# Performance work log

Hardware: AMD Instinct MI355X
Metric: run time of the kernel (lower is better)

## Reference

```python
import jax, jax.numpy as jnp
import numpy as np

N = 50000      # nodes
E = 1600000    # edges (avg degree 32)
D = 128        # node_feat_size
G = 128        # graph_feat_size (must equal D for BatchNorm1d to match MLP out)
EPS = 1e-5
NEG_SLOPE = 0.01  # LeakyReLU default


def setup_inputs() -> dict:
    key = jax.random.key(0)
    ks = jax.random.split(key, 10)
    p = lambda k, sh: jax.random.normal(k, sh, dtype=jnp.float32) * 0.05
    return {
        "node_feats": jax.random.normal(ks[0], (N, D), dtype=jnp.float32),
        "src": jax.random.randint(ks[1], (E,), 0, N, dtype=jnp.int32),
        "dst": jax.random.randint(ks[2], (E,), 0, N, dtype=jnp.int32),
        # project_edge: Linear(2D -> 1); split weight into dst/src halves
        "we_dst": p(ks[3], (D,)),
        "we_src": p(ks[4], (D,)),
        "be": jnp.zeros((), jnp.float32),
        # project_node: Linear(D -> G)
        "w_proj": p(ks[5], (D, G)),
        "b_proj": jnp.zeros((G,), jnp.float32),
        # MPL: Linear(G+D -> D), ReLU, Linear(D -> D)
        "w1": p(ks[6], (G + D, D)),
        "b1": jnp.zeros((D,), jnp.float32),
        "w2": p(ks[7], (D, D)),
        "b2": jnp.zeros((D,), jnp.float32),
        # BatchNorm1d(G) affine params (training-mode batch stats)
        "gamma": jnp.ones((G,), jnp.float32),
        "beta": jnp.zeros((G,), jnp.float32),
    }


def reference(node_feats, src, dst, we_dst, we_src, be, w_proj, b_proj,
              w1, b1, w2, b2, gamma, beta):
    # Edge logits: LeakyReLU(Linear(cat([dst_feat, src_feat])))
    # Linear over a concat == sum of two per-node projections -> avoid [E, 2D] tensor.
    ld = node_feats @ we_dst            # [N]
    ls = node_feats @ we_src            # [N]
    logit = ld[dst] + ls[src] + be      # [E]
    logit = jnp.where(logit >= 0, logit, NEG_SLOPE * logit)

    # edge_softmax: softmax over incoming edges of each destination node
    m = jax.ops.segment_max(logit, dst, num_segments=N)          # [N]
    ev = jnp.exp(logit - m[dst])                                  # [E]
    denom = jax.ops.segment_sum(ev, dst, num_segments=N)         # [N]
    a = ev / denom[dst]                                           # [E]

    # src_mul_edge + sum aggregation
    hv = node_feats @ w_proj + b_proj                             # [N, G]
    msg = hv[src] * a[:, None]                                    # [E, G]
    c = jax.ops.segment_sum(msg, dst, num_segments=N)             # [N, G]
    context = jax.nn.elu(c)

    # MPL: Linear -> ReLU -> Linear, then outer ReLU (dropout is identity in eval)
    h = jnp.concatenate([context, node_feats], axis=1)            # [N, G+D]
    h = jax.nn.relu(h @ w1 + b1)
    h = h @ w2 + b2
    h = jax.nn.relu(h)

    # BatchNorm1d in training mode: biased batch statistics
    mean = jnp.mean(h, axis=0)
    var = jnp.mean((h - mean) ** 2, axis=0)
    return gamma * (h - mean) / jnp.sqrt(var + EPS) + beta
```

## Files before the change

kernel.cpp:

```cpp
#include <hip/hip_runtime.h>
#include <math.h>

#define NN 50000
#define EE 1600000
#define DD 128
#define NB 98
#define SLAB 18432

typedef __attribute__((ext_vector_type(8))) short short8v;
typedef __attribute__((ext_vector_type(4))) float f32x4;
typedef __attribute__((ext_vector_type(2))) float floatx2;

#define HVB_OFF     0
#define CTXB_OFF    6400000
#define BIN_OFF     19200000
#define SRCS_OFF    26425344
#define LD_OFF      30038016
#define LS_OFF      30238016
#define START_OFF   30438016
#define CNTN_OFF    30638016
#define W1T_OFF     30838016
#define W2T_OFF     30903552
#define WPT_OFF     30936320
#define BKC_OFF     30969088
#define BSUM_OFF    30969600
#define BSQ_OFF     30970112
#define MEAN_OFF    30970624
#define ISTD_OFF    30971136
#define ZERO_OFF    BKC_OFF
#define ZERO_LEN    1536

__device__ __forceinline__ unsigned short f2bf(float f) {
  union { float f; unsigned u; } v; v.f = f;
  unsigned r = v.u + 0x7FFFu + ((v.u >> 16) & 1u);
  return (unsigned short)(r >> 16);
}

__global__ __launch_bounds__(256) void k_prep_w(const float* __restrict__ w1,
    const float* __restrict__ w2, const float* __restrict__ wp,
    unsigned short* __restrict__ w1t, unsigned short* __restrict__ w2t,
    unsigned short* __restrict__ wpt) {
  int t = blockIdx.x * 256 + threadIdx.x;
  if (t < 32768) {
    int n = t & 127, k = t >> 7;
    w1t[n * 256 + k] = f2bf(w1[(size_t)k * 128 + n]);
  } else if (t < 49152) {
    int i = t - 32768; int n = i & 127, k = i >> 7;
    w2t[n * 128 + k] = f2bf(w2[(size_t)k * 128 + n]);
  } else {
    int i = t - 49152; int n = i & 127, k = i >> 7;
    wpt[n * 128 + k] = f2bf(wp[(size_t)k * 128 + n]);
  }
}

__global__ __launch_bounds__(256) void k_hv2(const float* __restrict__ nf,
    const unsigned short* __restrict__ wpt, const float* __restrict__ bp,
    const float* __restrict__ wed, const float* __restrict__ wes,
    float* __restrict__ ld, float* __restrict__ ls,
    unsigned char* __restrict__ hvb) {
  __shared__ unsigned short xs[64][136];
  int tid = threadIdx.x;
  int m0 = blockIdx.x * 64;
  int c4 = tid & 31;
  float4 wdv = *(const float4*)(wed + c4 * 4);
  float4 wsv = *(const float4*)(wes + c4 * 4);
  #pragma unroll
  for (int e = 0; e < 8; ++e) {
    int idx = tid + 256 * e;
    int row = idx >> 5;
    int m = m0 + row;
    int mc = (m < NN) ? m : (NN - 1);
    float4 v = *(const float4*)(nf + (size_t)mc * 128 + c4 * 4);
    ushort4 bb;
    bb.x = f2bf(v.x); bb.y = f2bf(v.y); bb.z = f2bf(v.z); bb.w = f2bf(v.w);
    *(ushort4*)&xs[row][c4 * 4] = bb;
    float pa = v.x * wdv.x + v.y * wdv.y + v.z * wdv.z + v.w * wdv.w;
    float pb = v.x * wsv.x + v.y * wsv.y + v.z * wsv.z + v.w * wsv.w;
    #pragma unroll
    for (int o = 16; o; o >>= 1) { pa += __shfl_xor(pa, o); pb += __shfl_xor(pb, o); }
    if (c4 == 0 && m < NN) { ld[m] = pa; ls[m] = pb; }
  }
  __syncthreads();
  int wid = tid >> 6, lane = tid & 63;
  int wm = wid >> 1, wn = wid & 1;
  int l15 = lane & 15, lg = lane >> 4;
  f32x4 acc[4][2];
  #pragma unroll
  for (int nf2 = 0; nf2 < 4; ++nf2)
    #pragma unroll
    for (int mf = 0; mf < 2; ++mf) acc[nf2][mf] = (f32x4){0.f, 0.f, 0.f, 0.f};
  for (int ks = 0; ks < 4; ++ks) {
    short8v aw[4], bx[2];
    #pragma unroll
    for (int nf2 = 0; nf2 < 4; ++nf2) {
      int n = wn * 64 + nf2 * 16 + l15;
      aw[nf2] = *(const short8v*)(wpt + (size_t)n * 128 + ks * 32 + lg * 8);
    }
    #pragma unroll
    for (int mf = 0; mf < 2; ++mf)
      bx[mf] = *(const short8v*)&xs[wm * 32 + mf * 16 + l15][ks * 32 + lg * 8];
    #pragma unroll
    for (int nf2 = 0; nf2 < 4; ++nf2)
      #pragma unroll
      for (int mf = 0; mf < 2; ++mf)
        acc[nf2][mf] = __builtin_amdgcn_mfma_f32_16x16x32_bf16(aw[nf2], bx[mf], acc[nf2][mf], 0, 0, 0);
  }
  #pragma unroll
  for (int nf2 = 0; nf2 < 4; ++nf2) {
    float4 bp4 = *(const float4*)(bp + wn * 64 + nf2 * 16 + lg * 4);
    #pragma unroll
    for (int mf = 0; mf < 2; ++mf) {
      int m = m0 + wm * 32 + mf * 16 + l15;
      if (m < NN) {
        int w = __builtin_amdgcn_cvt_pk_fp8_f32(acc[nf2][mf][0] + bp4.x,
                                                acc[nf2][mf][1] + bp4.y, 0, false);
        w = __builtin_amdgcn_cvt_pk_fp8_f32(acc[nf2][mf][2] + bp4.z,
                                            acc[nf2][mf][3] + bp4.w, w, true);
        *(int*)(hvb + (size_t)m * 128 + wn * 64 + nf2 * 16 + lg * 4) = w;
      }
    }
  }
}

__global__ __launch_bounds__(256) void k_bin(const int* __restrict__ src,
    const int* __restrict__ dst, int* __restrict__ bkc,
    unsigned* __restrict__ bin) {
  __shared__ unsigned slot[8192];
  __shared__ int hist[128], sc[128], loff[128], lcur[128], gbase[128];
  int tid = threadIdx.x;
  int tbase = blockIdx.x * 8192;
  int tlen = min(8192, EE - tbase);
  unsigned pk[32];
  if (tid < 128) hist[tid] = 0;
  __syncthreads();
  #pragma unroll
  for (int k = 0; k < 32; ++k) {
    int i = k * 256 + tid;
    if (i < tlen) {
      int e = tbase + i;
      pk[k] = ((unsigned)dst[e] << 16) | (unsigned)src[e];
      atomicAdd(&hist[pk[k] >> 25], 1);
    }
  }
  __syncthreads();
  if (tid < 128) sc[tid] = hist[tid];
  __syncthreads();
  for (int off = 1; off < 128; off <<= 1) {
    int v = 0;
    if (tid < 128) v = sc[tid] + ((tid >= off) ? sc[tid - off] : 0);
    __syncthreads();
    if (tid < 128) sc[tid] = v;
    __syncthreads();
  }
  if (tid < 128) { loff[tid] = sc[tid] - hist[tid]; lcur[tid] = sc[tid] - hist[tid]; }
  __syncthreads();
  #pragma unroll
  for (int k = 0; k < 32; ++k) {
    int i = k * 256 + tid;
    if (i < tlen) {
      int r = atomicAdd(&lcur[pk[k] >> 25], 1);
      slot[r] = pk[k];
    }
  }
  __syncthreads();
  if (tid < 128) gbase[tid] = hist[tid] ? atomicAdd(&bkc[tid], hist[tid]) : 0;
  __syncthreads();
  #pragma unroll
  for (int k = 0; k < 32; ++k) {
    int i = k * 256 + tid;
    if (i < tlen) {
      unsigned p = slot[i];
      int b = p >> 25;
      bin[(size_t)b * SLAB + gbase[b] + (i - loff[b])] = p;
    }
  }
}

__global__ __launch_bounds__(256) void k_bsort(const unsigned* __restrict__ bin,
    const int* __restrict__ bkc, unsigned short* __restrict__ srcs,
    int* __restrict__ start, int* __restrict__ cntn) {
  __shared__ unsigned eL[SLAB];
  __shared__ unsigned short outL[SLAB];
  __shared__ int hist[512], scA[512], cur[512];
  int tid = threadIdx.x;
  int b = blockIdx.x;
  int base = b * SLAB;
  int cnt = bkc[b];
  int node0 = b << 9;
  int nnb = min(512, NN - node0);
  for (int i = tid; i < 512; i += 256) hist[i] = 0;
  __syncthreads();
  for (int i = tid; i < cnt; i += 256) {
    unsigned p = bin[base + i];
    eL[i] = p;
    atomicAdd(&hist[(p >> 16) & 511], 1);
  }
  __syncthreads();
  for (int i = tid; i < 512; i += 256) scA[i] = hist[i];
  __syncthreads();
  for (int off = 1; off < 512; off <<= 1) {
    int v0 = scA[tid] + ((tid >= off) ? scA[tid - off] : 0);
    int i1 = tid + 256;
    int v1 = scA[i1] + ((i1 >= off) ? scA[i1 - off] : 0);
    __syncthreads();
    scA[tid] = v0; scA[i1] = v1;
    __syncthreads();
  }
  for (int i = tid; i < 512; i += 256) {
    int ex = scA[i] - hist[i];
    cur[i] = ex;
    if (i < nnb) { start[node0 + i] = base + ex; cntn[node0 + i] = hist[i]; }
  }
  __syncthreads();
  for (int i = tid; i < cnt; i += 256) {
    unsigned p = eL[i];
    int r = atomicAdd(&cur[(p >> 16) & 511], 1);
    outL[r] = (unsigned short)(p & 0xFFFFu);
  }
  __syncthreads();
  for (int i = tid; i < cnt; i += 256) srcs[base + i] = outL[i];
}

__global__ __launch_bounds__(256) void k_agg(const unsigned char* __restrict__ hvb,
    const float* __restrict__ ld, const float* __restrict__ ls,
    const float* __restrict__ be_p, const int* __restrict__ start,
    const int* __restrict__ cntn, const unsigned short* __restrict__ srcs,
    unsigned short* __restrict__ ctxb) {
  int wid = (blockIdx.x * 256 + threadIdx.x) >> 6;
  int lane = threadIdx.x & 63;
  if (wid >= NN) return;
  int cnt = cntn[wid];
  int l8 = lane & 7, e8 = lane >> 3;
  float acc[16];
  #pragma unroll
  for (int i = 0; i < 16; ++i) acc[i] = 0.f;
  float m = -INFINITY, dsum = 0.f;
  if (cnt > 0) {
    int s = start[wid];
    float base = ld[wid] + be_p[0];
    for (int c0 = 0; c0 < cnt; c0 += 64) {
      int len = min(64, cnt - c0);
      float lg = -INFINITY;
      int sv = 0;
      if (lane < len) {
        sv = srcs[s + c0 + lane];
        float l = base + ls[sv];
        lg = (l >= 0.f) ? l : 0.01f * l;
      }
      float cm = lg;
      #pragma unroll
      for (int o = 32; o; o >>= 1) cm = fmaxf(cm, __shfl_xor(cm, o));
      float nm = fmaxf(m, cm);
      float sc = __expf(m - nm);
      #pragma unroll
      for (int i = 0; i < 16; ++i) acc[i] *= sc;
      dsum *= sc;
      float ev = (lane < len) ? __expf(lg - nm) : 0.f;
      dsum += ev;
      for (int j = 0; j < len; j += 8) {
        int jj = j + e8;
        float evj = __shfl(ev, jj);
        int svj = __shfl(sv, jj);
        if (jj < len) {
          uint4 U = *(const uint4*)(hvb + (size_t)svj * 128 + l8 * 16);
          floatx2 p;
          p = __builtin_amdgcn_cvt_pk_f32_fp8((int)U.x, false); acc[0] += evj * p[0];  acc[1] += evj * p[1];
          p = __builtin_amdgcn_cvt_pk_f32_fp8((int)U.x, true);  acc[2] += evj * p[0];  acc[3] += evj * p[1];
          p = __builtin_amdgcn_cvt_pk_f32_fp8((int)U.y, false); acc[4] += evj * p[0];  acc[5] += evj * p[1];
          p = __builtin_amdgcn_cvt_pk_f32_fp8((int)U.y, true);  acc[6] += evj * p[0];  acc[7] += evj * p[1];
          p = __builtin_amdgcn_cvt_pk_f32_fp8((int)U.z, false); acc[8] += evj * p[0];  acc[9] += evj * p[1];
          p = __builtin_amdgcn_cvt_pk_f32_fp8((int)U.z, true);  acc[10] += evj * p[0]; acc[11] += evj * p[1];
          p = __builtin_amdgcn_cvt_pk_f32_fp8((int)U.w, false); acc[12] += evj * p[0]; acc[13] += evj * p[1];
          p = __builtin_amdgcn_cvt_pk_f32_fp8((int)U.w, true);  acc[14] += evj * p[0]; acc[15] += evj * p[1];
        }
      }
      m = nm;
    }
  }
  #pragma unroll
  for (int o = 8; o <= 32; o <<= 1)
    #pragma unroll
    for (int i = 0; i < 16; ++i) acc[i] += __shfl_xor(acc[i], o);
  #pragma unroll
  for (int o = 32; o; o >>= 1) dsum += __shfl_xor(dsum, o);
  float r = (dsum > 0.f) ? (1.f / dsum) : 0.f;
  if (lane < 32) {
    int g = lane & 7, p4 = lane >> 3;
    float v0 = acc[p4 * 4 + 0] * r, v1 = acc[p4 * 4 + 1] * r;
    float v2 = acc[p4 * 4 + 2] * r, v3 = acc[p4 * 4 + 3] * r;
    v0 = (v0 > 0.f) ? v0 : expm1f(v0);
    v1 = (v1 > 0.f) ? v1 : expm1f(v1);
    v2 = (v2 > 0.f) ? v2 : expm1f(v2);
    v3 = (v3 > 0.f) ? v3 : expm1f(v3);
    uint2 u;
    u.x = (unsigned)f2bf(v0) | ((unsigned)f2bf(v1) << 16);
    u.y = (unsigned)f2bf(v2) | ((unsigned)f2bf(v3) << 16);
    *(uint2*)(ctxb + (size_t)wid * 128 + g * 16 + p4 * 4) = u;
  }
}

__global__ __launch_bounds__(256) void k_mlp2(const unsigned short* __restrict__ ctxb,
    const float* __restrict__ nf,
    const unsigned short* __restrict__ w1t, const float* __restrict__ b1,
    const unsigned short* __restrict__ w2t, const float* __restrict__ b2,
    float* __restrict__ out, float* __restrict__ bn_sum, float* __restrict__ bn_sumsq) {
  __shared__ unsigned short xs[64][264];
  __shared__ unsigned short h1s[64][136];
  __shared__ float bns[128], bnq[128];
  int tid = threadIdx.x;
  int m0 = blockIdx.x * 64;
  if (tid < 128) { bns[tid] = 0.f; bnq[tid] = 0.f; }
  #pragma unroll
  for (int e = 0; e < 4; ++e) {
    int idx = tid + 256 * e;
    int row = idx >> 4, c8 = idx & 15;
    int m = m0 + row; if (m >= NN) m = NN - 1;
    uint4 v = *(const uint4*)(ctxb + (size_t)m * 128 + c8 * 8);
    *(uint4*)&xs[row][c8 * 8] = v;
  }
  #pragma unroll
  for (int e = 0; e < 8; ++e) {
    int idx = tid + 256 * e;
    int row = idx >> 5, c4 = idx & 31;
    int m = m0 + row; if (m >= NN) m = NN - 1;
    float4 w = *(const float4*)(nf + (size_t)m * 128 + c4 * 4);
    ushort4 cc;
    cc.x = f2bf(w.x); cc.y = f2bf(w.y); cc.z = f2bf(w.z); cc.w = f2bf(w.w);
    *(ushort4*)&xs[row][128 + c4 * 4] = cc;
  }
  __syncthreads();
  int wid = tid >> 6, lane = tid & 63;
  int wm = wid >> 1, wn = wid & 1;
  int l15 = lane & 15, lg = lane >> 4;
  f32x4 acc[2][4];
  #pragma unroll
  for (int mf = 0; mf < 2; ++mf)
    #pragma unroll
    for (int nf2 = 0; nf2 < 4; ++nf2) acc[mf][nf2] = (f32x4){0.f, 0.f, 0.f, 0.f};
  for (int ks = 0; ks < 8; ++ks) {
    short8v a[2], b[4];
    #pragma unroll
    for (int mf = 0; mf < 2; ++mf)
      a[mf] = *(const short8v*)&xs[wm * 32 + mf * 16 + l15][ks * 32 + lg * 8];
    #pragma unroll
    for (int nf2 = 0; nf2 < 4; ++nf2) {
      int n = wn * 64 + nf2 * 16 + l15;
      b[nf2] = *(const short8v*)(w1t + (size_t)n * 256 + ks * 32 + lg * 8);
    }
    #pragma unroll
    for (int mf = 0; mf < 2; ++mf)
      #pragma unroll
      for (int nf2 = 0; nf2 < 4; ++nf2)
        acc[mf][nf2] = __builtin_amdgcn_mfma_f32_16x16x32_bf16(a[mf], b[nf2], acc[mf][nf2], 0, 0, 0);
  }
  {
    float b1n[4];
    #pragma unroll
    for (int nf2 = 0; nf2 < 4; ++nf2) b1n[nf2] = b1[wn * 64 + nf2 * 16 + l15];
    #pragma unroll
    for (int mf = 0; mf < 2; ++mf)
      #pragma unroll
      for (int nf2 = 0; nf2 < 4; ++nf2)
        #pragma unroll
        for (int r = 0; r < 4; ++r) {
          int row = wm * 32 + mf * 16 + lg * 4 + r;
          int col = wn * 64 + nf2 * 16 + l15;
          float h = fmaxf(acc[mf][nf2][r] + b1n[nf2], 0.f);
          h1s[row][col] = f2bf(h);
        }
  }
  __syncthreads();
  f32x4 acc2[2][4];
  #pragma unroll
  for (int mf = 0; mf < 2; ++mf)
    #pragma unroll
    for (int nf2 = 0; nf2 < 4; ++nf2) acc2[mf][nf2] = (f32x4){0.f, 0.f, 0.f, 0.f};
  for (int ks = 0; ks < 4; ++ks) {
    short8v a[2], b[4];
    #pragma unroll
    for (int mf = 0; mf < 2; ++mf)
      a[mf] = *(const short8v*)&h1s[wm * 32 + mf * 16 + l15][ks * 32 + lg * 8];
    #pragma unroll
    for (int nf2 = 0; nf2 < 4; ++nf2) {
      int n = wn * 64 + nf2 * 16 + l15;
      b[nf2] = *(const short8v*)(w2t + (size_t)n * 128 + ks * 32 + lg * 8);
    }
    #pragma unroll
    for (int mf = 0; mf < 2; ++mf)
      #pragma unroll
      for (int nf2 = 0; nf2 < 4; ++nf2)
        acc2[mf][nf2] = __builtin_amdgcn_mfma_f32_16x16x32_bf16(a[mf], b[nf2], acc2[mf][nf2], 0, 0, 0);
  }
  {
    float b2n[4];
    #pragma unroll
    for (int nf2 = 0; nf2 < 4; ++nf2) b2n[nf2] = b2[wn * 64 + nf2 * 16 + l15];
    float fsum[4] = {0.f, 0.f, 0.f, 0.f}, fsq[4] = {0.f, 0.f, 0.f, 0.f};
    #pragma unroll
    for (int mf = 0; mf < 2; ++mf)
      #pragma unroll
      for (int nf2 = 0; nf2 < 4; ++nf2)
        #pragma unroll
        for (int r = 0; r < 4; ++r) {
          int m = m0 + wm * 32 + mf * 16 + lg * 4 + r;
          int n = wn * 64 + nf2 * 16 + l15;
          float h = fmaxf(acc2[mf][nf2][r] + b2n[nf2], 0.f);
          if (m < NN) {
            out[(size_t)m * 128 + n] = h;
            fsum[nf2] += h;
            fsq[nf2] += h * h;
          }
        }
    #pragma unroll
    for (int nf2 = 0; nf2 < 4; ++nf2) {
      int n = wn * 64 + nf2 * 16 + l15;
      atomicAdd(&bns[n], fsum[nf2]);
      atomicAdd(&bnq[n], fsq[nf2]);
    }
  }
  __syncthreads();
  if (tid < 128) {
    atomicAdd(&bn_sum[tid], bns[tid]);
    atomicAdd(&bn_sumsq[tid], bnq[tid]);
  }
}

__global__ __launch_bounds__(128) void k_bnstats(const float* __restrict__ bn_sum,
    const float* __restrict__ bn_sumsq, float* __restrict__ mean,
    float* __restrict__ istd) {
  int t = threadIdx.x;
  float mu = bn_sum[t] / (float)NN;
  float var = bn_sumsq[t] / (float)NN - mu * mu;
  var = fmaxf(var, 0.f);
  mean[t] = mu;
  istd[t] = 1.f / sqrtf(var + 1e-5f);
}

__global__ __launch_bounds__(256) void k_bnorm(float* __restrict__ out,
    const float* __restrict__ mean, const float* __restrict__ istd,
    const float* __restrict__ gamma, const float* __restrict__ beta) {
  int idx = blockIdx.x * 256 + threadIdx.x;
  float4* p = (float4*)out;
  float4 v = p[idx];
  int f = (idx & 31) << 2;
  v.x = gamma[f + 0] * (v.x - mean[f + 0]) * istd[f + 0] + beta[f + 0];
  v.y = gamma[f + 1] * (v.y - mean[f + 1]) * istd[f + 1] + beta[f + 1];
  v.z = gamma[f + 2] * (v.z - mean[f + 2]) * istd[f + 2] + beta[f + 2];
  v.w = gamma[f + 3] * (v.w - mean[f + 3]) * istd[f + 3] + beta[f + 3];
  p[idx] = v;
}

extern "C" void kernel_launch(void* const* d_in, const int* in_sizes, int n_in,
                              void* d_out, int out_size, void* d_ws, size_t ws_size,
                              hipStream_t stream) {
  (void)in_sizes; (void)n_in; (void)out_size; (void)ws_size;
  const float* nf    = (const float*)d_in[0];
  const int*   src   = (const int*)d_in[1];
  const int*   dst   = (const int*)d_in[2];
  const float* wed   = (const float*)d_in[3];
  const float* wes   = (const float*)d_in[4];
  const float* be    = (const float*)d_in[5];
  const float* wp    = (const float*)d_in[6];
  const float* bp    = (const float*)d_in[7];
  const float* w1    = (const float*)d_in[8];
  const float* b1    = (const float*)d_in[9];
  const float* w2    = (const float*)d_in[10];
  const float* b2    = (const float*)d_in[11];
  const float* gamma = (const float*)d_in[12];
  const float* beta  = (const float*)d_in[13];
  float* out = (float*)d_out;
  char* ws = (char*)d_ws;

  unsigned char*  hvb  = (unsigned char*)(ws + HVB_OFF);
  unsigned short* ctxb = (unsigned short*)(ws + CTXB_OFF);
  unsigned*       bin  = (unsigned*)(ws + BIN_OFF);
  unsigned short* srcs = (unsigned short*)(ws + SRCS_OFF);
  float* ld    = (float*)(ws + LD_OFF);
  float* ls    = (float*)(ws + LS_OFF);
  int*   start = (int*)(ws + START_OFF);
  int*   cntn  = (int*)(ws + CNTN_OFF);
  unsigned short* w1t = (unsigned short*)(ws + W1T_OFF);
  unsigned short* w2t = (unsigned short*)(ws + W2T_OFF);
  unsigned short* wpt = (unsigned short*)(ws + WPT_OFF);
  int*   bkc   = (int*)(ws + BKC_OFF);
  float* bsum  = (float*)(ws + BSUM_OFF);
  float* bsq   = (float*)(ws + BSQ_OFF);
  float* mean  = (float*)(ws + MEAN_OFF);
  float* istd  = (float*)(ws + ISTD_OFF);

  hipMemsetAsync(ws + ZERO_OFF, 0, ZERO_LEN, stream);

  k_prep_w<<<256, 256, 0, stream>>>(w1, w2, wp, w1t, w2t, wpt);
  k_bin<<<196, 256, 0, stream>>>(src, dst, bkc, bin);
  k_hv2<<<(NN + 63) / 64, 256, 0, stream>>>(nf, wpt, bp, wed, wes, ld, ls, hvb);
  k_bsort<<<NB, 256, 0, stream>>>(bin, bkc, srcs, start, cntn);
  k_agg<<<12500, 256, 0, stream>>>(hvb, ld, ls, be, start, cntn, srcs, ctxb);
  k_mlp2<<<(NN + 63) / 64, 256, 0, stream>>>(ctxb, nf, w1t, b1, w2t, b2, out, bsum, bsq);
  k_bnstats<<<1, 128, 0, stream>>>(bsum, bsq, mean, istd);
  k_bnorm<<<(NN * DD / 4) / 256, 256, 0, stream>>>(out, mean, istd, gamma, beta);
}
```

Before: 288.9 us.

## Halve MLP tile rows, transpose second GEMM, write per-block BN partials

```diff
diff --git a/kernel.cpp b/kernel.cpp
--- a/kernel.cpp
+++ b/kernel.cpp
@@ -6,6 +6,8 @@
 #define DD 128
 #define NB 98
 #define SLAB 18432
+#define MROWS 32
+#define MGRID 1563
 
 typedef __attribute__((ext_vector_type(8))) short short8v;
 typedef __attribute__((ext_vector_type(4))) float f32x4;
@@ -23,12 +25,12 @@
 #define W2T_OFF     30903552
 #define WPT_OFF     30936320
 #define BKC_OFF     30969088
-#define BSUM_OFF    30969600
-#define BSQ_OFF     30970112
-#define MEAN_OFF    30970624
-#define ISTD_OFF    30971136
+#define MEAN_OFF    30969600
+#define ISTD_OFF    30970112
+#define PBN_OFF     30971648
+#define PBQ_OFF     31771904
 #define ZERO_OFF    BKC_OFF
-#define ZERO_LEN    1536
+#define ZERO_LEN    512
 
 __device__ __forceinline__ unsigned short f2bf(float f) {
   union { float f; unsigned u; } v; v.f = f;
@@ -303,15 +305,15 @@
     const float* __restrict__ nf,
     const unsigned short* __restrict__ w1t, const float* __restrict__ b1,
     const unsigned short* __restrict__ w2t, const float* __restrict__ b2,
-    float* __restrict__ out, float* __restrict__ bn_sum, float* __restrict__ bn_sumsq) {
-  __shared__ unsigned short xs[64][264];
-  __shared__ unsigned short h1s[64][136];
+    float* __restrict__ out, float* __restrict__ pbn, float* __restrict__ pbq) {
+  __shared__ unsigned short xs[MROWS][264];
+  __shared__ unsigned short h1s[MROWS][136];
   __shared__ float bns[128], bnq[128];
   int tid = threadIdx.x;
-  int m0 = blockIdx.x * 64;
+  int m0 = blockIdx.x * MROWS;
   if (tid < 128) { bns[tid] = 0.f; bnq[tid] = 0.f; }
   #pragma unroll
-  for (int e = 0; e < 4; ++e) {
+  for (int e = 0; e < 2; ++e) {
     int idx = tid + 256 * e;
     int row = idx >> 4, c8 = idx & 15;
     int m = m0 + row; if (m >= NN) m = NN - 1;
@@ -319,7 +321,7 @@
     *(uint4*)&xs[row][c8 * 8] = v;
   }
   #pragma unroll
-  for (int e = 0; e < 8; ++e) {
+  for (int e = 0; e < 4; ++e) {
     int idx = tid + 256 * e;
     int row = idx >> 5, c4 = idx & 31;
     int m = m0 + row; if (m >= NN) m = NN - 1;
@@ -332,108 +334,115 @@
   int wid = tid >> 6, lane = tid & 63;
   int wm = wid >> 1, wn = wid & 1;
   int l15 = lane & 15, lg = lane >> 4;
-  f32x4 acc[2][4];
-  #pragma unroll
-  for (int mf = 0; mf < 2; ++mf)
-    #pragma unroll
-    for (int nf2 = 0; nf2 < 4; ++nf2) acc[mf][nf2] = (f32x4){0.f, 0.f, 0.f, 0.f};
+  f32x4 acc[4];
+  #pragma unroll
+  for (int nf2 = 0; nf2 < 4; ++nf2) acc[nf2] = (f32x4){0.f, 0.f, 0.f, 0.f};
   for (int ks = 0; ks < 8; ++ks) {
-    short8v a[2], b[4];
-    #pragma unroll
-    for (int mf = 0; mf < 2; ++mf)
-      a[mf] = *(const short8v*)&xs[wm * 32 + mf * 16 + l15][ks * 32 + lg * 8];
+    short8v a = *(const short8v*)&xs[wm * 16 + l15][ks * 32 + lg * 8];
     #pragma unroll
     for (int nf2 = 0; nf2 < 4; ++nf2) {
       int n = wn * 64 + nf2 * 16 + l15;
-      b[nf2] = *(const short8v*)(w1t + (size_t)n * 256 + ks * 32 + lg * 8);
-    }
-    #pragma unroll
-    for (int mf = 0; mf < 2; ++mf)
-      #pragma unroll
-      for (int nf2 = 0; nf2 < 4; ++nf2)
-        acc[mf][nf2] = __builtin_amdgcn_mfma_f32_16x16x32_bf16(a[mf], b[nf2], acc[mf][nf2], 0, 0, 0);
+      short8v b = *(const short8v*)(w1t + (size_t)n * 256 + ks * 32 + lg * 8);
+      acc[nf2] = __builtin_amdgcn_mfma_f32_16x16x32_bf16(a, b, acc[nf2], 0, 0, 0);
+    }
   }
   {
     float b1n[4];
     #pragma unroll
     for (int nf2 = 0; nf2 < 4; ++nf2) b1n[nf2] = b1[wn * 64 + nf2 * 16 + l15];
     #pragma unroll
-    for (int mf = 0; mf < 2; ++mf)
+    for (int nf2 = 0; nf2 < 4; ++nf2)
+      #pragma unroll
+      for (int r = 0; r < 4; ++r) {
+        int row = wm * 16 + lg * 4 + r;
+        int col = wn * 64 + nf2 * 16 + l15;
+        h1s[row][col] = f2bf(fmaxf(acc[nf2][r] + b1n[nf2], 0.f));
+      }
+  }
+  __syncthreads();
+  f32x4 acc2[4];
+  #pragma unroll
+  for (int nf2 = 0; nf2 < 4; ++nf2) acc2[nf2] = (f32x4){0.f, 0.f, 0.f, 0.f};
+  for (int ks = 0; ks < 4; ++ks) {
+    short8v bh = *(const short8v*)&h1s[wm * 16 + l15][ks * 32 + lg * 8];
+    #pragma unroll
+    for (int nf2 = 0; nf2 < 4; ++nf2) {
+      int n = wn * 64 + nf2 * 16 + l15;
+      short8v aw = *(const short8v*)(w2t + (size_t)n * 128 + ks * 32 + lg * 8);
+      acc2[nf2] = __builtin_amdgcn_mfma_f32_16x16x32_bf16(aw, bh, acc2[nf2], 0, 0, 0);
+    }
+  }
+  {
+    int m = m0 + wm * 16 + l15;
+    bool valid = (m < NN);
+    float hs[4][4], hq[4][4];
+    #pragma unroll
+    for (int nf2 = 0; nf2 < 4; ++nf2) {
+      int f0 = wn * 64 + nf2 * 16 + lg * 4;
+      float4 b24 = *(const float4*)(b2 + f0);
+      float h0 = fmaxf(acc2[nf2][0] + b24.x, 0.f);
+      float h1v = fmaxf(acc2[nf2][1] + b24.y, 0.f);
+      float h2v = fmaxf(acc2[nf2][2] + b24.z, 0.f);
+      float h3v = fmaxf(acc2[nf2][3] + b24.w, 0.f);
+      if (valid) {
+        float4 o = make_float4(h0, h1v, h2v, h3v);
+        *(float4*)(out + (size_t)m * 128 + f0) = o;
+      } else { h0 = h1v = h2v = h3v = 0.f; }
+      hs[nf2][0] = h0; hs[nf2][1] = h1v; hs[nf2][2] = h2v; hs[nf2][3] = h3v;
+      hq[nf2][0] = h0 * h0; hq[nf2][1] = h1v * h1v;
+      hq[nf2][2] = h2v * h2v; hq[nf2][3] = h3v * h3v;
+    }
+    #pragma unroll
+    for (int o = 1; o <= 8; o <<= 1)
       #pragma unroll
       for (int nf2 = 0; nf2 < 4; ++nf2)
         #pragma unroll
         for (int r = 0; r < 4; ++r) {
-          int row = wm * 32 + mf * 16 + lg * 4 + r;
-          int col = wn * 64 + nf2 * 16 + l15;
-          float h = fmaxf(acc[mf][nf2][r] + b1n[nf2], 0.f);
-          h1s[row][col] = f2bf(h);
+          hs[nf2][r] += __shfl_xor(hs[nf2][r], o);
+          hq[nf2][r] += __shfl_xor(hq[nf2][r], o);
         }
-  }
-  __syncthreads();
-  f32x4 acc2[2][4];
-  #pragma unroll
-  for (int mf = 0; mf < 2; ++mf)
-    #pragma unroll
-    for (int nf2 = 0; nf2 < 4; ++nf2) acc2[mf][nf2] = (f32x4){0.f, 0.f, 0.f, 0.f};
-  for (int ks = 0; ks < 4; ++ks) {
-    short8v a[2], b[4];
-    #pragma unroll
-    for (int mf = 0; mf < 2; ++mf)
-      a[mf] = *(const short8v*)&h1s[wm * 32 + mf * 16 + l15][ks * 32 + lg * 8];
-    #pragma unroll
-    for (int nf2 = 0; nf2 < 4; ++nf2) {
-      int n = wn * 64 + nf2 * 16 + l15;
-      b[nf2] = *(const short8v*)(w2t + (size_t)n * 128 + ks * 32 + lg * 8);
-    }
-    #pragma unroll
-    for (int mf = 0; mf < 2; ++mf)
+    if (l15 == 0) {
       #pragma unroll
-      for (int nf2 = 0; nf2 < 4; ++nf2)
-        acc2[mf][nf2] = __builtin_amdgcn_mfma_f32_16x16x32_bf16(a[mf], b[nf2], acc2[mf][nf2], 0, 0, 0);
-  }
-  {
-    float b2n[4];
-    #pragma unroll
-    for (int nf2 = 0; nf2 < 4; ++nf2) b2n[nf2] = b2[wn * 64 + nf2 * 16 + l15];
-    float fsum[4] = {0.f, 0.f, 0.f, 0.f}, fsq[4] = {0.f, 0.f, 0.f, 0.f};
-    #pragma unroll
-    for (int mf = 0; mf < 2; ++mf)
-      #pragma unroll
-      for (int nf2 = 0; nf2 < 4; ++nf2)
+      for (int nf2 = 0; nf2 < 4; ++nf2) {
+        int f0 = wn * 64 + nf2 * 16 + lg * 4;
         #pragma unroll
         for (int r = 0; r < 4; ++r) {
-          int m = m0 + wm * 32 + mf * 16 + lg * 4 + r;
-          int n = wn * 64 + nf2 * 16 + l15;
-          float h = fmaxf(acc2[mf][nf2][r] + b2n[nf2], 0.f);
-          if (m < NN) {
-            out[(size_t)m * 128 + n] = h;
-            fsum[nf2] += h;
-            fsq[nf2] += h * h;
-          }
+          atomicAdd(&bns[f0 + r], hs[nf2][r]);
+          atomicAdd(&bnq[f0 + r], hq[nf2][r]);
         }
-    #pragma unroll
-    for (int nf2 = 0; nf2 < 4; ++nf2) {
-      int n = wn * 64 + nf2 * 16 + l15;
-      atomicAdd(&bns[n], fsum[nf2]);
-      atomicAdd(&bnq[n], fsq[nf2]);
+      }
     }
   }
   __syncthreads();
   if (tid < 128) {
-    atomicAdd(&bn_sum[tid], bns[tid]);
-    atomicAdd(&bn_sumsq[tid], bnq[tid]);
-  }
-}
-
-__global__ __launch_bounds__(128) void k_bnstats(const float* __restrict__ bn_sum,
-    const float* __restrict__ bn_sumsq, float* __restrict__ mean,
+    pbn[(size_t)blockIdx.x * 128 + tid] = bns[tid];
+    pbq[(size_t)blockIdx.x * 128 + tid] = bnq[tid];
+  }
+}
+
+__global__ __launch_bounds__(256) void k_bnstats2(const float* __restrict__ pbn,
+    const float* __restrict__ pbq, float* __restrict__ mean,
     float* __restrict__ istd) {
-  int t = threadIdx.x;
-  float mu = bn_sum[t] / (float)NN;
-  float var = bn_sumsq[t] / (float)NN - mu * mu;
-  var = fmaxf(var, 0.f);
-  mean[t] = mu;
-  istd[t] = 1.f / sqrtf(var + 1e-5f);
+  int f = blockIdx.x;
+  float s = 0.f, q = 0.f;
+  for (int b = threadIdx.x; b < MGRID; b += 256) {
+    s += pbn[(size_t)b * 128 + f];
+    q += pbq[(size_t)b * 128 + f];
+  }
+  #pragma unroll
+  for (int o = 32; o; o >>= 1) { s += __shfl_xor(s, o); q += __shfl_xor(q, o); }
+  __shared__ float ss[4], sq[4];
+  int wid = threadIdx.x >> 6, lane = threadIdx.x & 63;
+  if (lane == 0) { ss[wid] = s; sq[wid] = q; }
+  __syncthreads();
+  if (threadIdx.x == 0) {
+    float S = ss[0] + ss[1] + ss[2] + ss[3];
+    float Q = sq[0] + sq[1] + sq[2] + sq[3];
+    float mu = S / (float)NN;
+    float var = fmaxf(Q / (float)NN - mu * mu, 0.f);
+    mean[f] = mu;
+    istd[f] = 1.f / sqrtf(var + 1e-5f);
+  }
 }
 
 __global__ __launch_bounds__(256) void k_bnorm(float* __restrict__ out,
@@ -483,10 +492,10 @@
   unsigned short* w2t = (unsigned short*)(ws + W2T_OFF);
   unsigned short* wpt = (unsigned short*)(ws + WPT_OFF);
   int*   bkc   = (int*)(ws + BKC_OFF);
-  float* bsum  = (float*)(ws + BSUM_OFF);
-  float* bsq   = (float*)(ws + BSQ_OFF);
   float* mean  = (float*)(ws + MEAN_OFF);
   float* istd  = (float*)(ws + ISTD_OFF);
+  float* pbn   = (float*)(ws + PBN_OFF);
+  float* pbq   = (float*)(ws + PBQ_OFF);
 
   hipMemsetAsync(ws + ZERO_OFF, 0, ZERO_LEN, stream);
 
@@ -495,7 +504,7 @@
   k_hv2<<<(NN + 63) / 64, 256, 0, stream>>>(nf, wpt, bp, wed, wes, ld, ls, hvb);
   k_bsort<<<NB, 256, 0, stream>>>(bin, bkc, srcs, start, cntn);
   k_agg<<<12500, 256, 0, stream>>>(hvb, ld, ls, be, start, cntn, srcs, ctxb);
-  k_mlp2<<<(NN + 63) / 64, 256, 0, stream>>>(ctxb, nf, w1t, b1, w2t, b2, out, bsum, bsq);
-  k_bnstats<<<1, 128, 0, stream>>>(bsum, bsq, mean, istd);
+  k_mlp2<<<MGRID, 256, 0, stream>>>(ctxb, nf, w1t, b1, w2t, b2, out, pbn, pbq);
+  k_bnstats2<<<128, 256, 0, stream>>>(pbn, pbq, mean, istd);
   k_bnorm<<<(NN * DD / 4) / 256, 256, 0, stream>>>(out, mean, istd, gamma, beta);
 }
```

Measured after the change: 283.7 us. Within noise of the previous version (-1.8%).
